# Kernel optimization log

Measured on AMD Instinct MI355X. Metric: run time of the kernel, lower is better.

The kernel has to match this reference:

```python
import jax, jax.numpy as jnp
import numpy as np

N_USERS = 500_000
N_ITEMS = 200_000
D_FEAT = 256
H = 32
N_EDGES = 2_000_000
NEG_SLOPE = 0.01


def _lin(k, out_dim, in_dim):
    return jax.random.normal(k, (out_dim, in_dim), jnp.float32) * (1.0 / np.sqrt(in_dim))


def setup_inputs() -> dict:
    key = jax.random.key(0)
    ks = jax.random.split(key, 24)
    src = jax.random.randint(ks[0], (N_EDGES,), 0, N_USERS)   # user ids
    dst = jax.random.randint(ks[1], (N_EDGES,), 0, N_ITEMS)   # product ids
    inp = {
        "user_ids": jnp.arange(N_USERS, dtype=jnp.int32),
        "product_ids": jnp.arange(N_ITEMS, dtype=jnp.int32),
        "product_features": jax.random.normal(ks[2], (N_ITEMS, D_FEAT), jnp.float32),
        "edge_rates": jnp.stack([src, dst]),      # user -> product
        "edge_rated_by": jnp.stack([dst, src]),   # product -> user (reverse)
        "user_emb": jax.random.normal(ks[3], (N_USERS, H), jnp.float32),
        "item_emb": jax.random.normal(ks[4], (N_ITEMS, H), jnp.float32),
        "feat_W": _lin(ks[5], H, D_FEAT),
        "feat_b": jnp.zeros((H,), jnp.float32),
    }
    # SAGEConv params: lin_l (neighbor, with bias), lin_r (root, no bias)
    names = ["up1", "pu1", "up2", "pu2"]  # up = user->product conv, pu = product->user conv
    for i, n in enumerate(names):
        inp[f"Wl_{n}"] = _lin(ks[6 + 3 * i], H, H)
        inp[f"bl_{n}"] = jnp.zeros((H,), jnp.float32)
        inp[f"Wr_{n}"] = _lin(ks[7 + 3 * i], H, H)
    return inp


def _sage(x_src, x_dst, edge_index, Wl, bl, Wr):
    # PyG SAGEConv, aggr='mean': lin_l(mean_j x_src[j]) + lin_r(x_dst)
    e_src, e_dst = edge_index[0], edge_index[1]
    n_dst = x_dst.shape[0]
    msg_sum = jax.ops.segment_sum(x_src[e_src], e_dst, num_segments=n_dst)
    cnt = jax.ops.segment_sum(jnp.ones_like(e_dst, dtype=x_src.dtype), e_dst, num_segments=n_dst)
    mean = msg_sum / jnp.maximum(cnt, 1.0)[:, None]
    return mean @ Wl.T + bl + x_dst @ Wr.T


def reference(user_ids, product_ids, product_features, edge_rates, edge_rated_by,
              user_emb, item_emb, feat_W, feat_b,
              Wl_up1, bl_up1, Wr_up1, Wl_pu1, bl_pu1, Wr_pu1,
              Wl_up2, bl_up2, Wr_up2, Wl_pu2, bl_pu2, Wr_pu2):
    lrelu = lambda x: jax.nn.leaky_relu(x, NEG_SLOPE)
    xu = user_emb[user_ids]                                    # [Nu, H]
    xp = item_emb[product_ids] + product_features @ feat_W.T + feat_b  # [Ni, H]

    # layer 1 (HeteroConv: each node type has exactly one incoming relation)
    p1 = lrelu(_sage(xu, xp, edge_rates, Wl_up1, bl_up1, Wr_up1))
    u1 = lrelu(_sage(xp, xu, edge_rated_by, Wl_pu1, bl_pu1, Wr_pu1))
    # layer 2
    p2 = lrelu(_sage(u1, p1, edge_rates, Wl_up2, bl_up2, Wr_up2))
    u2 = lrelu(_sage(p1, u1, edge_rated_by, Wl_pu2, bl_pu2, Wr_pu2))

    final_user = jnp.concatenate([xu, u1, u2], axis=1)   # [Nu, 3H]
    final_item = jnp.concatenate([xp, p1, p2], axis=1)   # [Ni, 3H]
    return final_user, final_item
```

## Files before the change

### kernel.cpp

```cpp
#include <hip/hip_runtime.h>

#define NU 500000
#define NI 200000
#define NN (NU + NI)
#define NE 2000000
#define HD 32
#define DF 256
#define OC 96

typedef float        f4  __attribute__((ext_vector_type(4)));
typedef unsigned int u2  __attribute__((ext_vector_type(2)));
typedef unsigned int u4v __attribute__((ext_vector_type(4)));
typedef short        s8v __attribute__((ext_vector_type(8)));
typedef unsigned short ushort_t;

__device__ __forceinline__ float lrelu(float v){ return v >= 0.f ? v : 0.01f*v; }

__device__ __forceinline__ unsigned int f2bf(float f){
  unsigned int u = __float_as_uint(f);
  u += 0x7fffu + ((u >> 16) & 1u);
  return u >> 16;
}
__device__ __forceinline__ float bflo(unsigned int u){ return __uint_as_float(u << 16); }
__device__ __forceinline__ float bfhi(unsigned int u){ return __uint_as_float(u & 0xffff0000u); }

__device__ __forceinline__ s8v pack8(f4 a, f4 b){
  s8v r;
  r[0]=(short)f2bf(a.x); r[1]=(short)f2bf(a.y); r[2]=(short)f2bf(a.z); r[3]=(short)f2bf(a.w);
  r[4]=(short)f2bf(b.x); r[5]=(short)f2bf(b.y); r[6]=(short)f2bf(b.z); r[7]=(short)f2bf(b.w);
  return r;
}

__global__ void k_deg(const int* __restrict__ esrc, const int* __restrict__ edst,
                      int* __restrict__ cnt){
  int e = blockIdx.x*blockDim.x + threadIdx.x;
  if (e >= NE) return;
  int u = __builtin_nontemporal_load(esrc + e);
  int p = __builtin_nontemporal_load(edst + e);
  atomicAdd(cnt + u, 1);
  atomicAdd(cnt + NU + p, 1);
}

__global__ void k_init_user(const int* __restrict__ ids, const float* __restrict__ emb,
                            float* __restrict__ outu, ushort_t* __restrict__ tbl){
  int tid = blockIdx.x*256 + threadIdx.x;
  int node = tid >> 3;
  if (node >= NU) return;
  int q = tid & 7;
  int uid = ids[node];
  f4 v = *((const f4*)(emb + (size_t)uid*HD) + q);
  __builtin_nontemporal_store(v, (f4*)(outu + (size_t)node*OC) + q);
  u2 pv; pv.x = f2bf(v.x) | (f2bf(v.y) << 16); pv.y = f2bf(v.z) | (f2bf(v.w) << 16);
  ((u2*)tbl)[(size_t)node*8 + q] = pv;
}

__global__ __launch_bounds__(256) void k_init_item_mfma(
    const int* __restrict__ ids, const float* __restrict__ emb,
    const float* __restrict__ feat, const float* __restrict__ W,
    const float* __restrict__ bias, float* __restrict__ outi){
  int wave = threadIdx.x >> 6;
  int lane = threadIdx.x & 63;
  int tile = blockIdx.x*4 + wave;
  int row0 = tile*16;
  if (row0 >= NI) return;
  int m = lane & 15, grp = lane >> 4;

  s8v bfrag[16];
  #pragma unroll
  for (int ks = 0; ks < 8; ++ks) {
    #pragma unroll
    for (int nh = 0; nh < 2; ++nh) {
      const float* wp = W + (size_t)(nh*16 + m)*DF + ks*32 + grp*8;
      f4 w0 = *(const f4*)wp;
      f4 w1 = *(const f4*)(wp + 4);
      bfrag[ks*2 + nh] = pack8(w0, w1);
    }
  }

  f4 acc0 = {0,0,0,0}, acc1 = {0,0,0,0};
  const float* fr = feat + (size_t)(row0 + m)*DF + grp*8;
  #pragma unroll
  for (int ks = 0; ks < 8; ++ks) {
    f4 a0 = *(const f4*)(fr + ks*32);
    f4 a1 = *(const f4*)(fr + ks*32 + 4);
    s8v af = pack8(a0, a1);
    acc0 = __builtin_amdgcn_mfma_f32_16x16x32_bf16(af, bfrag[ks*2+0], acc0, 0, 0, 0);
    acc1 = __builtin_amdgcn_mfma_f32_16x16x32_bf16(af, bfrag[ks*2+1], acc1, 0, 0, 0);
  }

  #pragma unroll
  for (int j = 0; j < 4; ++j) {
    int r = row0 + grp*4 + j;
    int pid = ids[r];
    float v0 = acc0[j] + emb[(size_t)pid*HD + m]      + bias[m];
    float v1 = acc1[j] + emb[(size_t)pid*HD + 16 + m] + bias[16 + m];
    outi[(size_t)r*OC + m]      = v0;
    outi[(size_t)r*OC + 16 + m] = v1;
  }
}

__global__ void k_tbl_item(const float* __restrict__ outi, ushort_t* __restrict__ tbl){
  int tid = blockIdx.x*256 + threadIdx.x;
  int node = tid >> 3;
  if (node >= NI) return;
  int q = tid & 7;
  f4 v = *((const f4*)(outi + (size_t)node*OC) + q);
  u2 pv; pv.x = f2bf(v.x) | (f2bf(v.y) << 16); pv.y = f2bf(v.z) | (f2bf(v.w) << 16);
  ((u2*)tbl)[(size_t)node*8 + q] = pv;
}

__global__ void k_push(const ushort_t* __restrict__ tbl,
                       const int* __restrict__ eS, const int* __restrict__ eD,
                       ushort_t* __restrict__ acc){
  int tid = blockIdx.x*256 + threadIdx.x;
  int e = tid >> 3;
  if (e >= NE) return;
  int q = tid & 7;
  int s = __builtin_nontemporal_load(eS + e);
  int d = __builtin_nontemporal_load(eD + e);
  u2 v = ((const u2*)tbl)[(size_t)s*8 + q];
  ushort_t* a = acc + (size_t)d*HD + q*4;
  asm volatile("global_atomic_pk_add_bf16 %0, %1, off"          :: "v"(a), "v"(v.x) : "memory");
  asm volatile("global_atomic_pk_add_bf16 %0, %1, off offset:4" :: "v"(a), "v"(v.y) : "memory");
}

__global__ void k_fin3(float* __restrict__ dstbase, int n,
                       const ushort_t* __restrict__ acc, const int* __restrict__ cnt,
                       const ushort_t* __restrict__ xtbl, int outoff,
                       const float* __restrict__ Wl, const float* __restrict__ bl,
                       const float* __restrict__ Wr, ushort_t* __restrict__ tblout){
  int i = blockIdx.x*blockDim.x + threadIdx.x;
  if (i >= n) return;
  int c = cnt[i];
  float inv = (c > 0) ? 1.f/(float)c : 0.f;
  float m[HD], x[HD];
  const u4v* ar = (const u4v*)(acc + (size_t)i*HD);
  const u4v* xr = (const u4v*)(xtbl + (size_t)i*HD);
  #pragma unroll
  for (int t = 0; t < 4; ++t) {
    u4v v = ar[t];
    m[8*t+0] = bflo(v.x)*inv; m[8*t+1] = bfhi(v.x)*inv;
    m[8*t+2] = bflo(v.y)*inv; m[8*t+3] = bfhi(v.y)*inv;
    m[8*t+4] = bflo(v.z)*inv; m[8*t+5] = bfhi(v.z)*inv;
    m[8*t+6] = bflo(v.w)*inv; m[8*t+7] = bfhi(v.w)*inv;
    u4v xv = xr[t];
    x[8*t+0] = bflo(xv.x); x[8*t+1] = bfhi(xv.x);
    x[8*t+2] = bflo(xv.y); x[8*t+3] = bfhi(xv.y);
    x[8*t+4] = bflo(xv.z); x[8*t+5] = bfhi(xv.z);
    x[8*t+6] = bflo(xv.w); x[8*t+7] = bfhi(xv.w);
  }
  float y[HD];
  #pragma unroll
  for (int h = 0; h < HD; ++h) {
    float s = bl[h];
    #pragma unroll
    for (int j = 0; j < HD; ++j) s += m[j]*Wl[h*HD+j];
    #pragma unroll
    for (int j = 0; j < HD; ++j) s += x[j]*Wr[h*HD+j];
    y[h] = lrelu(s);
  }
  float* row = dstbase + (size_t)i*OC + outoff;
  #pragma unroll
  for (int qq = 0; qq < 8; ++qq) {
    f4 yo; yo.x=y[4*qq+0]; yo.y=y[4*qq+1]; yo.z=y[4*qq+2]; yo.w=y[4*qq+3];
    __builtin_nontemporal_store(yo, (f4*)row + qq);
  }
  if (tblout) {
    u4v pv[4];
    #pragma unroll
    for (int t = 0; t < 4; ++t) {
      pv[t].x = f2bf(y[8*t+0]) | (f2bf(y[8*t+1]) << 16);
      pv[t].y = f2bf(y[8*t+2]) | (f2bf(y[8*t+3]) << 16);
      pv[t].z = f2bf(y[8*t+4]) | (f2bf(y[8*t+5]) << 16);
      pv[t].w = f2bf(y[8*t+6]) | (f2bf(y[8*t+7]) << 16);
    }
    u4v* tb = (u4v*)(tblout + (size_t)i*HD);
    #pragma unroll
    for (int t = 0; t < 4; ++t) tb[t] = pv[t];
  }
}

extern "C" void kernel_launch(void* const* d_in, const int* in_sizes, int n_in,
                              void* d_out, int out_size, void* d_ws, size_t ws_size,
                              hipStream_t stream) {
  const int*   user_ids = (const int*)d_in[0];
  const int*   prod_ids = (const int*)d_in[1];
  const float* feat     = (const float*)d_in[2];
  const int*   er       = (const int*)d_in[3];
  const float* uemb     = (const float*)d_in[5];
  const float* iemb     = (const float*)d_in[6];
  const float* fW       = (const float*)d_in[7];
  const float* fb       = (const float*)d_in[8];
  const float* Wl_up1 = (const float*)d_in[9];
  const float* bl_up1 = (const float*)d_in[10];
  const float* Wr_up1 = (const float*)d_in[11];
  const float* Wl_pu1 = (const float*)d_in[12];
  const float* bl_pu1 = (const float*)d_in[13];
  const float* Wr_pu1 = (const float*)d_in[14];
  const float* Wl_up2 = (const float*)d_in[15];
  const float* bl_up2 = (const float*)d_in[16];
  const float* Wr_up2 = (const float*)d_in[17];
  const float* Wl_pu2 = (const float*)d_in[18];
  const float* bl_pu2 = (const float*)d_in[19];
  const float* Wr_pu2 = (const float*)d_in[20];

  float* outu = (float*)d_out;
  float* outi = outu + (size_t)NU*OC;

  char* w = (char*)d_ws;
  int* cnt = (int*)w;                         w += ((size_t)NN*4 + 255) & ~(size_t)255;
  ushort_t* tblU  = (ushort_t*)w;             w += (size_t)NU*HD*2;
  ushort_t* tblI  = (ushort_t*)w;             w += (size_t)NI*HD*2;
  ushort_t* tblU2 = (ushort_t*)w;             w += (size_t)NU*HD*2;
  ushort_t* tblI2 = (ushort_t*)w;             w += (size_t)NI*HD*2;
  ushort_t* accU  = (ushort_t*)w;             w += (size_t)NU*HD*2;
  ushort_t* accI  = (ushort_t*)w;

  const int* er_src = er;
  const int* er_dst = er + NE;

  const int B = 256;
  const int GE  = (NE + B - 1)/B;
  const int GE8 = ((size_t)NE*8 + B - 1)/B;
  const int GU8 = ((size_t)NU*8 + B - 1)/B, GI8 = ((size_t)NI*8 + B - 1)/B;
  const int GU1 = (NU + B - 1)/B,           GI1 = (NI + B - 1)/B;
  const size_t accU_bytes = (size_t)NU*HD*2, accI_bytes = (size_t)NI*HD*2;

  hipMemsetAsync(cnt, 0, (size_t)NN*4, stream);
  k_deg<<<GE, B, 0, stream>>>(er_src, er_dst, cnt);

  k_init_user<<<GU8, B, 0, stream>>>(user_ids, uemb, outu, tblU);
  k_init_item_mfma<<<(NI + 63)/64, 256, 0, stream>>>(prod_ids, iemb, feat, fW, fb, outi);
  k_tbl_item<<<GI8, B, 0, stream>>>(outi, tblI);

  hipMemsetAsync(accI, 0, accI_bytes, stream);
  k_push<<<GE8, B, 0, stream>>>(tblU, er_src, er_dst, accI);
  k_fin3<<<GI1, B, 0, stream>>>(outi, NI, accI, cnt + NU, tblI, 32,
                                Wl_up1, bl_up1, Wr_up1, tblI2);
  hipMemsetAsync(accU, 0, accU_bytes, stream);
  k_push<<<GE8, B, 0, stream>>>(tblI, er_dst, er_src, accU);
  k_fin3<<<GU1, B, 0, stream>>>(outu, NU, accU, cnt, tblU, 32,
                                Wl_pu1, bl_pu1, Wr_pu1, tblU2);
  hipMemsetAsync(accI, 0, accI_bytes, stream);
  k_push<<<GE8, B, 0, stream>>>(tblU2, er_src, er_dst, accI);
  k_fin3<<<GI1, B, 0, stream>>>(outi, NI, accI, cnt + NU, tblI2, 64,
                                Wl_up2, bl_up2, Wr_up2, (ushort_t*)nullptr);
  hipMemsetAsync(accU, 0, accU_bytes, stream);
  k_push<<<GE8, B, 0, stream>>>(tblI2, er_dst, er_src, accU);
  k_fin3<<<GU1, B, 0, stream>>>(outu, NU, accU, cnt, tblU2, 64,
                                Wl_pu2, bl_pu2, Wr_pu2, (ushort_t*)nullptr);
}
```

Measured before the change: 1.943 ms.

## Accumulate neighbor sums in fp32 directly in output rows, drop scratch buffers

Neighbor sums are now accumulated with fp32 atomics straight into the output rows, in the slot each layer later overwrites, rather than into separate bf16 accumulator buffers. Init kernels zero those slots, so the memsets go, and the item init writes the bf16 table itself, removing k_tbl_item. The finalize kernel reads the mean and root features from the fp32 output rows instead of the bf16 tables. The cost is four scalar fp32 atomics per thread where there were two packed bf16 atomics, which doubles atomic traffic, in exchange for fewer passes and better accumulation precision.

```diff
diff --git a/kernel.cpp b/kernel.cpp
--- a/kernel.cpp
+++ b/kernel.cpp
@@ -29,6 +29,11 @@
   r[0]=(short)f2bf(a.x); r[1]=(short)f2bf(a.y); r[2]=(short)f2bf(a.z); r[3]=(short)f2bf(a.w);
   r[4]=(short)f2bf(b.x); r[5]=(short)f2bf(b.y); r[6]=(short)f2bf(b.z); r[7]=(short)f2bf(b.w);
   return r;
+}
+
+__global__ void k_zero_i32(int* __restrict__ p, int n){
+  int i = blockIdx.x*blockDim.x + threadIdx.x;
+  if (i < n) p[i] = 0;
 }
 
 __global__ void k_deg(const int* __restrict__ esrc, const int* __restrict__ edst,
@@ -43,21 +48,35 @@
 
 __global__ void k_init_user(const int* __restrict__ ids, const float* __restrict__ emb,
                             float* __restrict__ outu, ushort_t* __restrict__ tbl){
-  int tid = blockIdx.x*256 + threadIdx.x;
-  int node = tid >> 3;
-  if (node >= NU) return;
-  int q = tid & 7;
-  int uid = ids[node];
-  f4 v = *((const f4*)(emb + (size_t)uid*HD) + q);
-  __builtin_nontemporal_store(v, (f4*)(outu + (size_t)node*OC) + q);
-  u2 pv; pv.x = f2bf(v.x) | (f2bf(v.y) << 16); pv.y = f2bf(v.z) | (f2bf(v.w) << 16);
-  ((u2*)tbl)[(size_t)node*8 + q] = pv;
+  int i = blockIdx.x*blockDim.x + threadIdx.x;
+  if (i >= NU) return;
+  int uid = ids[i];
+  const f4* s = (const f4*)(emb + (size_t)uid*HD);
+  f4* d = (f4*)(outu + (size_t)i*OC);
+  unsigned int pk[16];
+  #pragma unroll
+  for (int q = 0; q < 8; ++q) {
+    f4 v = s[q];
+    __builtin_nontemporal_store(v, d + q);
+    pk[2*q]   = f2bf(v.x) | (f2bf(v.y) << 16);
+    pk[2*q+1] = f2bf(v.z) | (f2bf(v.w) << 16);
+  }
+  f4 z = {0,0,0,0};
+  #pragma unroll
+  for (int q = 8; q < 24; ++q) __builtin_nontemporal_store(z, d + q);
+  u4v* t = (u4v*)(tbl + (size_t)i*HD);
+  #pragma unroll
+  for (int q = 0; q < 4; ++q) {
+    u4v v; v.x = pk[4*q]; v.y = pk[4*q+1]; v.z = pk[4*q+2]; v.w = pk[4*q+3];
+    t[q] = v;
+  }
 }
 
 __global__ __launch_bounds__(256) void k_init_item_mfma(
     const int* __restrict__ ids, const float* __restrict__ emb,
     const float* __restrict__ feat, const float* __restrict__ W,
-    const float* __restrict__ bias, float* __restrict__ outi){
+    const float* __restrict__ bias, float* __restrict__ outi,
+    ushort_t* __restrict__ tbl){
   int wave = threadIdx.x >> 6;
   int lane = threadIdx.x & 63;
   int tile = blockIdx.x*4 + wave;
@@ -88,6 +107,7 @@
     acc1 = __builtin_amdgcn_mfma_f32_16x16x32_bf16(af, bfrag[ks*2+1], acc1, 0, 0, 0);
   }
 
+  f4 z = {0,0,0,0};
   #pragma unroll
   for (int j = 0; j < 4; ++j) {
     int r = row0 + grp*4 + j;
@@ -96,58 +116,45 @@
     float v1 = acc1[j] + emb[(size_t)pid*HD + 16 + m] + bias[16 + m];
     outi[(size_t)r*OC + m]      = v0;
     outi[(size_t)r*OC + 16 + m] = v1;
-  }
-}
-
-__global__ void k_tbl_item(const float* __restrict__ outi, ushort_t* __restrict__ tbl){
-  int tid = blockIdx.x*256 + threadIdx.x;
-  int node = tid >> 3;
-  if (node >= NI) return;
-  int q = tid & 7;
-  f4 v = *((const f4*)(outi + (size_t)node*OC) + q);
-  u2 pv; pv.x = f2bf(v.x) | (f2bf(v.y) << 16); pv.y = f2bf(v.z) | (f2bf(v.w) << 16);
-  ((u2*)tbl)[(size_t)node*8 + q] = pv;
+    __builtin_nontemporal_store(z, (f4*)(outi + (size_t)r*OC + 32 + 4*m));
+    tbl[(size_t)r*HD + m]      = (ushort_t)f2bf(v0);
+    tbl[(size_t)r*HD + 16 + m] = (ushort_t)f2bf(v1);
+  }
 }
 
 __global__ void k_push(const ushort_t* __restrict__ tbl,
                        const int* __restrict__ eS, const int* __restrict__ eD,
-                       ushort_t* __restrict__ acc){
+                       float* __restrict__ outbase, int accoff){
   int tid = blockIdx.x*256 + threadIdx.x;
   int e = tid >> 3;
   if (e >= NE) return;
   int q = tid & 7;
-  int s = __builtin_nontemporal_load(eS + e);
-  int d = __builtin_nontemporal_load(eD + e);
+  int s = eS[e];
+  int d = eD[e];
   u2 v = ((const u2*)tbl)[(size_t)s*8 + q];
-  ushort_t* a = acc + (size_t)d*HD + q*4;
-  asm volatile("global_atomic_pk_add_bf16 %0, %1, off"          :: "v"(a), "v"(v.x) : "memory");
-  asm volatile("global_atomic_pk_add_bf16 %0, %1, off offset:4" :: "v"(a), "v"(v.y) : "memory");
-}
-
-__global__ void k_fin3(float* __restrict__ dstbase, int n,
-                       const ushort_t* __restrict__ acc, const int* __restrict__ cnt,
-                       const ushort_t* __restrict__ xtbl, int outoff,
-                       const float* __restrict__ Wl, const float* __restrict__ bl,
-                       const float* __restrict__ Wr, ushort_t* __restrict__ tblout){
+  float* a = outbase + (size_t)d*OC + accoff + q*4;
+  atomicAdd(a + 0, bflo(v.x));
+  atomicAdd(a + 1, bfhi(v.x));
+  atomicAdd(a + 2, bflo(v.y));
+  atomicAdd(a + 3, bfhi(v.y));
+}
+
+__global__ void k_fin(float* __restrict__ base, int n, int accoff, int xoff,
+                      const int* __restrict__ cnt,
+                      const float* __restrict__ Wl, const float* __restrict__ bl,
+                      const float* __restrict__ Wr, ushort_t* __restrict__ tblout){
   int i = blockIdx.x*blockDim.x + threadIdx.x;
   if (i >= n) return;
+  float* row = base + (size_t)i*OC;
   int c = cnt[i];
   float inv = (c > 0) ? 1.f/(float)c : 0.f;
   float m[HD], x[HD];
-  const u4v* ar = (const u4v*)(acc + (size_t)i*HD);
-  const u4v* xr = (const u4v*)(xtbl + (size_t)i*HD);
-  #pragma unroll
-  for (int t = 0; t < 4; ++t) {
-    u4v v = ar[t];
-    m[8*t+0] = bflo(v.x)*inv; m[8*t+1] = bfhi(v.x)*inv;
-    m[8*t+2] = bflo(v.y)*inv; m[8*t+3] = bfhi(v.y)*inv;
-    m[8*t+4] = bflo(v.z)*inv; m[8*t+5] = bfhi(v.z)*inv;
-    m[8*t+6] = bflo(v.w)*inv; m[8*t+7] = bfhi(v.w)*inv;
-    u4v xv = xr[t];
-    x[8*t+0] = bflo(xv.x); x[8*t+1] = bfhi(xv.x);
-    x[8*t+2] = bflo(xv.y); x[8*t+3] = bfhi(xv.y);
-    x[8*t+4] = bflo(xv.z); x[8*t+5] = bfhi(xv.z);
-    x[8*t+6] = bflo(xv.w); x[8*t+7] = bfhi(xv.w);
+  #pragma unroll
+  for (int q = 0; q < 8; ++q) {
+    f4 a = *((const f4*)(row + accoff) + q);
+    m[4*q+0]=a.x*inv; m[4*q+1]=a.y*inv; m[4*q+2]=a.z*inv; m[4*q+3]=a.w*inv;
+    f4 xx = *((const f4*)(row + xoff) + q);
+    x[4*q+0]=xx.x; x[4*q+1]=xx.y; x[4*q+2]=xx.z; x[4*q+3]=xx.w;
   }
   float y[HD];
   #pragma unroll
@@ -159,11 +166,10 @@
     for (int j = 0; j < HD; ++j) s += x[j]*Wr[h*HD+j];
     y[h] = lrelu(s);
   }
-  float* row = dstbase + (size_t)i*OC + outoff;
-  #pragma unroll
-  for (int qq = 0; qq < 8; ++qq) {
-    f4 yo; yo.x=y[4*qq+0]; yo.y=y[4*qq+1]; yo.z=y[4*qq+2]; yo.w=y[4*qq+3];
-    __builtin_nontemporal_store(yo, (f4*)row + qq);
+  #pragma unroll
+  for (int q = 0; q < 8; ++q) {
+    f4 yo; yo.x=y[4*q+0]; yo.y=y[4*q+1]; yo.z=y[4*q+2]; yo.w=y[4*q+3];
+    *((f4*)(row + accoff) + q) = yo;
   }
   if (tblout) {
     u4v pv[4];
@@ -208,45 +214,35 @@
   float* outi = outu + (size_t)NU*OC;
 
   char* w = (char*)d_ws;
-  int* cnt = (int*)w;                         w += ((size_t)NN*4 + 255) & ~(size_t)255;
-  ushort_t* tblU  = (ushort_t*)w;             w += (size_t)NU*HD*2;
-  ushort_t* tblI  = (ushort_t*)w;             w += (size_t)NI*HD*2;
-  ushort_t* tblU2 = (ushort_t*)w;             w += (size_t)NU*HD*2;
-  ushort_t* tblI2 = (ushort_t*)w;             w += (size_t)NI*HD*2;
-  ushort_t* accU  = (ushort_t*)w;             w += (size_t)NU*HD*2;
-  ushort_t* accI  = (ushort_t*)w;
+  int* cnt = (int*)w;              w += ((size_t)NN*4 + 255) & ~(size_t)255;
+  ushort_t* tblU  = (ushort_t*)w;  w += (size_t)NU*HD*2;
+  ushort_t* tblI  = (ushort_t*)w;  w += (size_t)NI*HD*2;
+  ushort_t* tblU2 = (ushort_t*)w;  w += (size_t)NU*HD*2;
+  ushort_t* tblI2 = (ushort_t*)w;
 
   const int* er_src = er;
   const int* er_dst = er + NE;
 
   const int B = 256;
   const int GE  = (NE + B - 1)/B;
-  const int GE8 = ((size_t)NE*8 + B - 1)/B;
-  const int GU8 = ((size_t)NU*8 + B - 1)/B, GI8 = ((size_t)NI*8 + B - 1)/B;
-  const int GU1 = (NU + B - 1)/B,           GI1 = (NI + B - 1)/B;
-  const size_t accU_bytes = (size_t)NU*HD*2, accI_bytes = (size_t)NI*HD*2;
-
-  hipMemsetAsync(cnt, 0, (size_t)NN*4, stream);
+  const int GE8 = (int)(((size_t)NE*8 + B - 1)/B);
+  const int GU1 = (NU + B - 1)/B, GI1 = (NI + B - 1)/B;
+
+  k_zero_i32<<<(NN + B - 1)/B, B, 0, stream>>>(cnt, NN);
   k_deg<<<GE, B, 0, stream>>>(er_src, er_dst, cnt);
 
-  k_init_user<<<GU8, B, 0, stream>>>(user_ids, uemb, outu, tblU);
-  k_init_item_mfma<<<(NI + 63)/64, 256, 0, stream>>>(prod_ids, iemb, feat, fW, fb, outi);
-  k_tbl_item<<<GI8, B, 0, stream>>>(outi, tblI);
-
-  hipMemsetAsync(accI, 0, accI_bytes, stream);
-  k_push<<<GE8, B, 0, stream>>>(tblU, er_src, er_dst, accI);
-  k_fin3<<<GI1, B, 0, stream>>>(outi, NI, accI, cnt + NU, tblI, 32,
-                                Wl_up1, bl_up1, Wr_up1, tblI2);
-  hipMemsetAsync(accU, 0, accU_bytes, stream);
-  k_push<<<GE8, B, 0, stream>>>(tblI, er_dst, er_src, accU);
-  k_fin3<<<GU1, B, 0, stream>>>(outu, NU, accU, cnt, tblU, 32,
-                                Wl_pu1, bl_pu1, Wr_pu1, tblU2);
-  hipMemsetAsync(accI, 0, accI_bytes, stream);
-  k_push<<<GE8, B, 0, stream>>>(tblU2, er_src, er_dst, accI);
-  k_fin3<<<GI1, B, 0, stream>>>(outi, NI, accI, cnt + NU, tblI2, 64,
-                                Wl_up2, bl_up2, Wr_up2, (ushort_t*)nullptr);
-  hipMemsetAsync(accU, 0, accU_bytes, stream);
-  k_push<<<GE8, B, 0, stream>>>(tblI2, er_dst, er_src, accU);
-  k_fin3<<<GU1, B, 0, stream>>>(outu, NU, accU, cnt, tblU2, 64,
-                                Wl_pu2, bl_pu2, Wr_pu2, (ushort_t*)nullptr);
-}
+  k_init_user<<<GU1, B, 0, stream>>>(user_ids, uemb, outu, tblU);
+  k_init_item_mfma<<<(NI + 63)/64, 256, 0, stream>>>(prod_ids, iemb, feat, fW, fb,
+                                                     outi, tblI);
+
+  k_push<<<GE8, B, 0, stream>>>(tblU, er_src, er_dst, outi, 32);
+  k_fin<<<GI1, B, 0, stream>>>(outi, NI, 32, 0, cnt + NU, Wl_up1, bl_up1, Wr_up1, tblI2);
+  k_push<<<GE8, B, 0, stream>>>(tblI, er_dst, er_src, outu, 32);
+  k_fin<<<GU1, B, 0, stream>>>(outu, NU, 32, 0, cnt, Wl_pu1, bl_pu1, Wr_pu1, tblU2);
+  k_push<<<GE8, B, 0, stream>>>(tblU2, er_src, er_dst, outi, 64);
+  k_fin<<<GI1, B, 0, stream>>>(outi, NI, 64, 32, cnt + NU, Wl_up2, bl_up2, Wr_up2,
+                               (ushort_t*)nullptr);
+  k_push<<<GE8, B, 0, stream>>>(tblI2, er_dst, er_src, outu, 64);
+  k_fin<<<GU1, B, 0, stream>>>(outu, NU, 64, 32, cnt, Wl_pu2, bl_pu2, Wr_pu2,
+                               (ushort_t*)nullptr);
+}
```

Measured after the change: 4.301 ms. +121.4%, slower.
